# Optimization experiments

Hardware: AMD Instinct MI355X
Metric: run time of the kernel (lower is better)

## Reference

```python
import jax, jax.numpy as jnp
import numpy as np

BITS = 4
GROUP = 128
MAXQ = 2 ** BITS - 1  # 15 for asymmetric 4-bit


def round_ste(x):
    # straight-through rounding: round in fwd, identity in bwd
    return x + jax.lax.stop_gradient(jnp.round(x) - x)


def quant_weight(weight, v, min_scale, max_scale):
    """Groupwise asymmetric fake-quant (quantize + dequantize) of weight.

    weight: [O, I], v: [O, I] learnable rounding offsets,
    min_scale/max_scale: [O*I/GROUP] learnable min/max scales in [-1, 0].
    """
    O, I = weight.shape
    w = weight.reshape(-1, GROUP)          # [G, GROUP]
    vv = v.reshape(-1, GROUP)              # [G, GROUP]
    wmin_t = jnp.minimum(w.min(axis=1), 0.0)  # [G]
    wmax_t = jnp.maximum(w.max(axis=1), 0.0)  # [G]
    # forward clamps min/max scale into [-1, 0] before use
    wmin = wmin_t * (jnp.clip(min_scale, -1.0, 0.0) + 1.0)
    wmax = wmax_t * (jnp.clip(max_scale, -1.0, 0.0) + 1.0)
    degenerate = (wmin == 0.0) & (wmax == 0.0)
    wmin = jnp.where(degenerate, -1.0, wmin)
    wmax = jnp.where(degenerate, 1.0, wmax)
    # scale stored at fp16 precision (scale_dtype), then used in fp32 math
    scale = ((wmax - wmin) / MAXQ).astype(jnp.float16).astype(weight.dtype)  # [G]
    zp = round_ste(-wmin / scale)                                            # [G]
    int_w = round_ste(w / scale[:, None] + vv)                               # [G, GROUP]
    q = jnp.clip(int_w + zp[:, None], 0.0, float(MAXQ))
    wq = scale[:, None] * (q - zp[:, None])
    return wq.reshape(O, I)


def setup_inputs() -> dict:
    key = jax.random.key(0)
    k_x, k_w, k_b, k_v = jax.random.split(key, 4)
    O, I = 4096, 4096
    B, S = 2, 2048
    x = jax.random.normal(k_x, (B, S, I), dtype=jnp.float32)
    weight = jax.random.normal(k_w, (O, I), dtype=jnp.float32) * 0.02
    bias = jax.random.normal(k_b, (O,), dtype=jnp.float32) * 0.02
    value = jax.random.normal(k_v, (O, I), dtype=jnp.float32) * 0.1
    n_groups = O * I // GROUP
    min_scale = jnp.zeros((n_groups,), dtype=jnp.float32)
    max_scale = jnp.zeros((n_groups,), dtype=jnp.float32)
    return {"x": x, "weight": weight, "bias": bias, "value": value,
            "min_scale": min_scale, "max_scale": max_scale}


def reference(x, weight, bias, value, min_scale, max_scale):
    wq = quant_weight(weight, value, min_scale, max_scale)  # [O, I]
    # F.linear(x, weight_q, bias): x @ wq.T + bias
    return jnp.einsum('bsi,oi->bso', x, wq) + bias
```

## Files before the change

### kernel.cpp

```cpp
#include <hip/hip_runtime.h>
#include <hip/hip_bf16.h>
#include <hip/hip_fp16.h>
#include <stdint.h>

#define M_DIM 4096
#define N_DIM 4096
#define K_DIM 4096
#define GROUPSZ 128
#define MAXQ 15.0f

#define BM 256
#define BN 256
#define BK 64
#define T_TILES (K_DIM / BK)

typedef __attribute__((ext_vector_type(8))) short short8;
typedef __attribute__((ext_vector_type(4))) float f32x4;

__global__ __launch_bounds__(256) void quant_kernel(
    const float* __restrict__ weight, const float* __restrict__ value,
    const float* __restrict__ min_scale, const float* __restrict__ max_scale,
    __hip_bfloat16* __restrict__ wq)
{
    const int tid  = threadIdx.x;
    const int wave = tid >> 6;
    const int lane = tid & 63;
    const long g    = (long)blockIdx.x * 4 + wave;
    const long base = g * GROUPSZ + lane * 2;

    const float2 w = *(const float2*)(weight + base);
    const float2 v = *(const float2*)(value  + base);

    float mn = fminf(w.x, w.y);
    float mx = fmaxf(w.x, w.y);
#pragma unroll
    for (int off = 32; off >= 1; off >>= 1) {
        mn = fminf(mn, __shfl_xor(mn, off, 64));
        mx = fmaxf(mx, __shfl_xor(mx, off, 64));
    }
    mn = fminf(mn, 0.0f);
    mx = fmaxf(mx, 0.0f);

    const float ms = fminf(fmaxf(min_scale[g], -1.0f), 0.0f) + 1.0f;
    const float xs = fminf(fmaxf(max_scale[g], -1.0f), 0.0f) + 1.0f;
    float wmin = mn * ms;
    float wmax = mx * xs;
    if (wmin == 0.0f && wmax == 0.0f) { wmin = -1.0f; wmax = 1.0f; }

    const float scale = (float)(_Float16)((wmax - wmin) / MAXQ);
    const float zp    = rintf(-wmin / scale);

    const float q0 = fminf(fmaxf(rintf(w.x / scale + v.x) + zp, 0.0f), MAXQ);
    const float q1 = fminf(fmaxf(rintf(w.y / scale + v.y) + zp, 0.0f), MAXQ);
    const float o0 = scale * (q0 - zp);
    const float o1 = scale * (q1 - zp);

    __hip_bfloat162 o;
    o.x = __float2bfloat16(o0);
    o.y = __float2bfloat16(o1);
    *(__hip_bfloat162*)(wq + base) = o;
}

__global__ __launch_bounds__(256) void cast_kernel(
    const float* __restrict__ x, __hip_bfloat16* __restrict__ xb)
{
    const long i = ((long)blockIdx.x * 256 + threadIdx.x) * 8;
    const float4 a = *(const float4*)(x + i);
    const float4 b = *(const float4*)(x + i + 4);
    union { short8 s; __hip_bfloat16 h[8]; } u;
    u.h[0] = __float2bfloat16(a.x);
    u.h[1] = __float2bfloat16(a.y);
    u.h[2] = __float2bfloat16(a.z);
    u.h[3] = __float2bfloat16(a.w);
    u.h[4] = __float2bfloat16(b.x);
    u.h[5] = __float2bfloat16(b.y);
    u.h[6] = __float2bfloat16(b.z);
    u.h[7] = __float2bfloat16(b.w);
    *(short8*)(xb + i) = u.s;
}

__global__ __launch_bounds__(512, 2) void gemm_kernel(
    const __hip_bfloat16* __restrict__ A,
    const __hip_bfloat16* __restrict__ B,
    const float* __restrict__ bias,
    float* __restrict__ C)
{
    __shared__ __align__(16) char lds[131072];

    const int tid  = threadIdx.x;
    const int lane = tid & 63;
    const int wv   = tid >> 6;
    const int wm   = wv >> 2;
    const int wn   = wv & 3;

    const int bid = blockIdx.x;
    const int swz = (bid & 7) * (gridDim.x >> 3) + (bid >> 3);
    const int brow = (swz >> 4) * BM;
    const int bcol = (swz & 15) * BN;

    const int stg_r = tid >> 3;
    const int cc    = ((tid & 7) ^ (stg_r & 7)) * 8;

#define STAGE(XP, rowbase, h, tau, ldsbase)                                         \
    { _Pragma("unroll")                                                             \
      for (int inst = 0; inst < 2; ++inst) {                                        \
        const __hip_bfloat16* g = (XP) +                                            \
            (size_t)((rowbase) + (h) * 128 + inst * 64 + stg_r) * K_DIM +           \
            (tau) * 64 + cc;                                                        \
        __builtin_amdgcn_global_load_lds(                                           \
            (const __attribute__((address_space(1))) void*)g,                       \
            (__attribute__((address_space(3))) void*)(lds + (ldsbase) +             \
                (h) * 16384 + inst * 8192 + (wv << 10)),                            \
            16, 0, 0);                                                              \
      } }

    const int ro = lane & 15;
    const int hi = lane >> 4;
    const int slot0 = ((0 + hi) ^ (ro & 7)) << 4;
    const int slot1 = ((4 + hi) ^ (ro & 7)) << 4;
    const int rbA = (wm * 128 + ro) * 128;
    const int rbB = (wn * 64  + ro) * 128;

    f32x4 acc[8][4] = {};

    STAGE(B, bcol, 0, 0, 65536);
    STAGE(B, bcol, 1, 0, 65536);
    STAGE(A, brow, 0, 0, 0);
    STAGE(A, brow, 1, 0, 0);
    STAGE(B, bcol, 0, 1, 65536 + 32768);
    STAGE(B, bcol, 1, 1, 65536 + 32768);
    asm volatile("s_waitcnt vmcnt(4)" ::: "memory");
    __builtin_amdgcn_s_barrier();

#define MFMA16(M0, XA0, XA1)                                                        \
    { _Pragma("unroll")                                                             \
      for (int n = 0; n < 4; ++n) {                                                 \
        acc[M0][n]     = __builtin_amdgcn_mfma_f32_16x16x32_bf16((XA0)[0], bfr[n][0], acc[M0][n],     0, 0, 0); \
        acc[M0 + 1][n] = __builtin_amdgcn_mfma_f32_16x16x32_bf16((XA1)[0], bfr[n][0], acc[M0 + 1][n], 0, 0, 0); \
      }                                                                             \
      _Pragma("unroll")                                                             \
      for (int n = 0; n < 4; ++n) {                                                 \
        acc[M0][n]     = __builtin_amdgcn_mfma_f32_16x16x32_bf16((XA0)[1], bfr[n][1], acc[M0][n],     0, 0, 0); \
        acc[M0 + 1][n] = __builtin_amdgcn_mfma_f32_16x16x32_bf16((XA1)[1], bfr[n][1], acc[M0 + 1][n], 0, 0, 0); \
      } }

#define LD_A(dst, m)                                                                \
    dst[0] = *(const short8*)(bA + (m) * 2048 + slot0);                             \
    dst[1] = *(const short8*)(bA + (m) * 2048 + slot1);

    for (int t = 0; t < T_TILES; ++t) {
        const int c = t & 1;
        const char* bA = lds + c * 32768 + rbA;
        const char* bB = lds + 65536 + c * 32768 + rbB;

        short8 bfr[4][2];
        short8 x0[2], x1[2];

#pragma unroll
        for (int n = 0; n < 4; ++n) {
            bfr[n][0] = *(const short8*)(bB + n * 2048 + slot0);
            bfr[n][1] = *(const short8*)(bB + n * 2048 + slot1);
        }
        LD_A(x0, 0); LD_A(x1, 1);
        if (t + 1 < T_TILES) {
            STAGE(A, brow, 0, t + 1, (c ^ 1) * 32768);
            STAGE(A, brow, 1, t + 1, (c ^ 1) * 32768);
        }
        asm volatile("s_waitcnt lgkmcnt(8)" ::: "memory");
        __builtin_amdgcn_s_barrier();
        asm volatile("s_waitcnt lgkmcnt(0)" ::: "memory");
        __builtin_amdgcn_s_setprio(1);
        MFMA16(0, x0, x1);
        __builtin_amdgcn_s_setprio(0);
        __builtin_amdgcn_s_barrier();

        LD_A(x0, 2); LD_A(x1, 3);
        if (t + 2 < T_TILES) { STAGE(B, bcol, 0, t + 2, 65536 + c * 32768); }
        __builtin_amdgcn_s_barrier();
        asm volatile("s_waitcnt lgkmcnt(0)" ::: "memory");
        __builtin_amdgcn_s_setprio(1);
        MFMA16(2, x0, x1);
        __builtin_amdgcn_s_setprio(0);
        __builtin_amdgcn_s_barrier();

        LD_A(x0, 4); LD_A(x1, 5);
        if (t + 2 < T_TILES) { STAGE(B, bcol, 1, t + 2, 65536 + c * 32768); }
        __builtin_amdgcn_s_barrier();
        asm volatile("s_waitcnt lgkmcnt(0)" ::: "memory");
        __builtin_amdgcn_s_setprio(1);
        MFMA16(4, x0, x1);
        __builtin_amdgcn_s_setprio(0);
        __builtin_amdgcn_s_barrier();

        LD_A(x0, 6); LD_A(x1, 7);
        if (t < T_TILES - 2) { asm volatile("s_waitcnt vmcnt(4)" ::: "memory"); }
        else                 { asm volatile("s_waitcnt vmcnt(0)" ::: "memory"); }
        __builtin_amdgcn_s_barrier();
        asm volatile("s_waitcnt lgkmcnt(0)" ::: "memory");
        __builtin_amdgcn_s_setprio(1);
        MFMA16(6, x0, x1);
        __builtin_amdgcn_s_setprio(0);
        __builtin_amdgcn_s_barrier();
    }

    const int col   = lane & 15;
    const int rbase = hi * 4;
    float bv[4];
#pragma unroll
    for (int n = 0; n < 4; ++n)
        bv[n] = bias[bcol + wn * 64 + n * 16 + col];

#pragma unroll
    for (int m = 0; m < 8; ++m) {
        const int mrow = brow + wm * 128 + m * 16 + rbase;
#pragma unroll
        for (int r = 0; r < 4; ++r) {
            float* crow = C + (size_t)(mrow + r) * N_DIM + bcol + wn * 64 + col;
#pragma unroll
            for (int n = 0; n < 4; ++n)
                crow[n * 16] = acc[m][n][r] + bv[n];
        }
    }
#undef STAGE
#undef MFMA16
#undef LD_A
}

extern "C" void kernel_launch(void* const* d_in, const int* in_sizes, int n_in,
                              void* d_out, int out_size, void* d_ws, size_t ws_size,
                              hipStream_t stream) {
    const float* x         = (const float*)d_in[0];
    const float* weight    = (const float*)d_in[1];
    const float* bias      = (const float*)d_in[2];
    const float* value     = (const float*)d_in[3];
    const float* min_scale = (const float*)d_in[4];
    const float* max_scale = (const float*)d_in[5];
    float* out = (float*)d_out;

    __hip_bfloat16* xb  = (__hip_bfloat16*)d_ws;
    __hip_bfloat16* wqb = xb + (size_t)M_DIM * K_DIM;

    quant_kernel<<<(N_DIM * K_DIM / GROUPSZ) / 4, 256, 0, stream>>>(
        weight, value, min_scale, max_scale, wqb);
    cast_kernel<<<(M_DIM * K_DIM) / (256 * 8), 256, 0, stream>>>(x, xb);
    gemm_kernel<<<(M_DIM / BM) * (N_DIM / BN), 512, 0, stream>>>(xb, wqb, bias, out);
}
```

Baseline: 172.3 us.

## Software-pipeline LDS fragment loads across MFMA phases with register double buffering

Restructures the GEMM main loop so that the B fragments and first A fragments for the next K tile are read from LDS during the current tile's last MFMA phase. The A fragments for each phase are loaded one phase ahead. The loop is unrolled by two with ping-pong register sets, and several barriers and full lgkmcnt(0) waits are replaced by partial waits. The goal is to hide LDS read latency behind MFMA work and cut synchronisation stalls. The cost is higher VGPR pressure and more fragile waitcnt and barrier ordering around the async global-to-LDS stages.

```diff
diff --git a/kernel.cpp b/kernel.cpp
--- a/kernel.cpp
+++ b/kernel.cpp
@@ -122,6 +122,24 @@
     const int rbB = (wn * 64  + ro) * 128;
 
     f32x4 acc[8][4] = {};
+    short8 bR0[4][2], bR1[4][2];
+    short8 aP0[2][2], aP1[2][2];
+
+#define MFMA16(M0, BIN, X0, X1)                                                     \
+    { _Pragma("unroll")                                                             \
+      for (int n = 0; n < 4; ++n) {                                                 \
+        acc[M0][n]     = __builtin_amdgcn_mfma_f32_16x16x32_bf16((X0)[0], BIN[n][0], acc[M0][n],     0, 0, 0); \
+        acc[M0 + 1][n] = __builtin_amdgcn_mfma_f32_16x16x32_bf16((X1)[0], BIN[n][0], acc[M0 + 1][n], 0, 0, 0); \
+      }                                                                             \
+      _Pragma("unroll")                                                             \
+      for (int n = 0; n < 4; ++n) {                                                 \
+        acc[M0][n]     = __builtin_amdgcn_mfma_f32_16x16x32_bf16((X0)[1], BIN[n][1], acc[M0][n],     0, 0, 0); \
+        acc[M0 + 1][n] = __builtin_amdgcn_mfma_f32_16x16x32_bf16((X1)[1], BIN[n][1], acc[M0 + 1][n], 0, 0, 0); \
+      } }
+
+#define LDA2(dst, m)                                                                \
+    dst[0] = *(const short8*)(bA_ + (m) * 2048 + slot0);                            \
+    dst[1] = *(const short8*)(bA_ + (m) * 2048 + slot1);
 
     STAGE(B, bcol, 0, 0, 65536);
     STAGE(B, bcol, 1, 0, 65536);
@@ -131,76 +149,76 @@
     STAGE(B, bcol, 1, 1, 65536 + 32768);
     asm volatile("s_waitcnt vmcnt(4)" ::: "memory");
     __builtin_amdgcn_s_barrier();
-
-#define MFMA16(M0, XA0, XA1)                                                        \
-    { _Pragma("unroll")                                                             \
-      for (int n = 0; n < 4; ++n) {                                                 \
-        acc[M0][n]     = __builtin_amdgcn_mfma_f32_16x16x32_bf16((XA0)[0], bfr[n][0], acc[M0][n],     0, 0, 0); \
-        acc[M0 + 1][n] = __builtin_amdgcn_mfma_f32_16x16x32_bf16((XA1)[0], bfr[n][0], acc[M0 + 1][n], 0, 0, 0); \
-      }                                                                             \
-      _Pragma("unroll")                                                             \
-      for (int n = 0; n < 4; ++n) {                                                 \
-        acc[M0][n]     = __builtin_amdgcn_mfma_f32_16x16x32_bf16((XA0)[1], bfr[n][1], acc[M0][n],     0, 0, 0); \
-        acc[M0 + 1][n] = __builtin_amdgcn_mfma_f32_16x16x32_bf16((XA1)[1], bfr[n][1], acc[M0 + 1][n], 0, 0, 0); \
-      } }
-
-#define LD_A(dst, m)                                                                \
-    dst[0] = *(const short8*)(bA + (m) * 2048 + slot0);                             \
-    dst[1] = *(const short8*)(bA + (m) * 2048 + slot1);
-
-    for (int t = 0; t < T_TILES; ++t) {
-        const int c = t & 1;
-        const char* bA = lds + c * 32768 + rbA;
-        const char* bB = lds + 65536 + c * 32768 + rbB;
-
-        short8 bfr[4][2];
-        short8 x0[2], x1[2];
-
+    {
+        const char* bB_ = lds + 65536 + rbB;
+        const char* bA_ = lds + rbA;
 #pragma unroll
         for (int n = 0; n < 4; ++n) {
-            bfr[n][0] = *(const short8*)(bB + n * 2048 + slot0);
-            bfr[n][1] = *(const short8*)(bB + n * 2048 + slot1);
+            bR0[n][0] = *(const short8*)(bB_ + n * 2048 + slot0);
+            bR0[n][1] = *(const short8*)(bB_ + n * 2048 + slot1);
         }
-        LD_A(x0, 0); LD_A(x1, 1);
-        if (t + 1 < T_TILES) {
-            STAGE(A, brow, 0, t + 1, (c ^ 1) * 32768);
-            STAGE(A, brow, 1, t + 1, (c ^ 1) * 32768);
-        }
-        asm volatile("s_waitcnt lgkmcnt(8)" ::: "memory");
-        __builtin_amdgcn_s_barrier();
-        asm volatile("s_waitcnt lgkmcnt(0)" ::: "memory");
-        __builtin_amdgcn_s_setprio(1);
-        MFMA16(0, x0, x1);
-        __builtin_amdgcn_s_setprio(0);
-        __builtin_amdgcn_s_barrier();
-
-        LD_A(x0, 2); LD_A(x1, 3);
-        if (t + 2 < T_TILES) { STAGE(B, bcol, 0, t + 2, 65536 + c * 32768); }
-        __builtin_amdgcn_s_barrier();
-        asm volatile("s_waitcnt lgkmcnt(0)" ::: "memory");
-        __builtin_amdgcn_s_setprio(1);
-        MFMA16(2, x0, x1);
-        __builtin_amdgcn_s_setprio(0);
-        __builtin_amdgcn_s_barrier();
-
-        LD_A(x0, 4); LD_A(x1, 5);
-        if (t + 2 < T_TILES) { STAGE(B, bcol, 1, t + 2, 65536 + c * 32768); }
-        __builtin_amdgcn_s_barrier();
-        asm volatile("s_waitcnt lgkmcnt(0)" ::: "memory");
-        __builtin_amdgcn_s_setprio(1);
-        MFMA16(4, x0, x1);
-        __builtin_amdgcn_s_setprio(0);
-        __builtin_amdgcn_s_barrier();
-
-        LD_A(x0, 6); LD_A(x1, 7);
-        if (t < T_TILES - 2) { asm volatile("s_waitcnt vmcnt(4)" ::: "memory"); }
-        else                 { asm volatile("s_waitcnt vmcnt(0)" ::: "memory"); }
-        __builtin_amdgcn_s_barrier();
-        asm volatile("s_waitcnt lgkmcnt(0)" ::: "memory");
-        __builtin_amdgcn_s_setprio(1);
-        MFMA16(6, x0, x1);
-        __builtin_amdgcn_s_setprio(0);
-        __builtin_amdgcn_s_barrier();
+        LDA2(aP0[0], 0); LDA2(aP0[1], 1);
+    }
+
+#define TILE_BODY(T_, BIN, BOUT, AIN, AOUT)                                         \
+    {                                                                               \
+        const int t_ = (T_);                                                        \
+        const int c_ = t_ & 1;                                                      \
+        const char* bA_  = lds + c_ * 32768 + rbA;                                  \
+        const char* bAn_ = lds + (c_ ^ 1) * 32768 + rbA;                            \
+        const char* bBn_ = lds + 65536 + (c_ ^ 1) * 32768 + rbB;                    \
+        short8 a23[2][2], a45[2][2], a67[2][2];                                     \
+                                                                            \
+        LDA2(a23[0], 2); LDA2(a23[1], 3);                                           \
+        if (t_ + 1 < T_TILES) {                                                     \
+            STAGE(A, brow, 0, t_ + 1, (c_ ^ 1) * 32768);                            \
+            STAGE(A, brow, 1, t_ + 1, (c_ ^ 1) * 32768);                            \
+        }                                                                           \
+        asm volatile("s_waitcnt lgkmcnt(4)" ::: "memory");                          \
+        __builtin_amdgcn_s_setprio(1);                                              \
+        MFMA16(0, BIN, AIN[0], AIN[1]);                                             \
+        __builtin_amdgcn_s_setprio(0);                                              \
+        __builtin_amdgcn_s_barrier();                                               \
+                                                                            \
+        LDA2(a45[0], 4); LDA2(a45[1], 5);                                           \
+        if (t_ + 2 < T_TILES) { STAGE(B, bcol, 0, t_ + 2, 65536 + c_ * 32768); }    \
+        asm volatile("s_waitcnt lgkmcnt(4)" ::: "memory");                          \
+        __builtin_amdgcn_s_setprio(1);                                              \
+        MFMA16(2, BIN, a23[0], a23[1]);                                             \
+        __builtin_amdgcn_s_setprio(0);                                              \
+        __builtin_amdgcn_s_barrier();                                               \
+                                                                            \
+        LDA2(a67[0], 6); LDA2(a67[1], 7);                                           \
+        if (t_ + 2 < T_TILES) { STAGE(B, bcol, 1, t_ + 2, 65536 + c_ * 32768); }    \
+        asm volatile("s_waitcnt lgkmcnt(4)" ::: "memory");                          \
+        __builtin_amdgcn_s_setprio(1);                                              \
+        MFMA16(4, BIN, a45[0], a45[1]);                                             \
+        __builtin_amdgcn_s_setprio(0);                                              \
+        if (t_ + 2 < T_TILES)      { asm volatile("s_waitcnt vmcnt(4)" ::: "memory"); } \
+        else if (t_ + 1 < T_TILES) { asm volatile("s_waitcnt vmcnt(0)" ::: "memory"); } \
+        __builtin_amdgcn_s_barrier();                                               \
+                                                                            \
+        if (t_ + 1 < T_TILES) {                                                     \
+            _Pragma("unroll")                                                       \
+            for (int n = 0; n < 4; ++n) {                                           \
+                BOUT[n][0] = *(const short8*)(bBn_ + n * 2048 + slot0);             \
+                BOUT[n][1] = *(const short8*)(bBn_ + n * 2048 + slot1);             \
+            }                                                                       \
+            { const char* bA_ = bAn_;                                               \
+              LDA2(AOUT[0], 0); LDA2(AOUT[1], 1); }                                 \
+            asm volatile("s_waitcnt lgkmcnt(12)" ::: "memory");                     \
+        } else {                                                                    \
+            asm volatile("s_waitcnt lgkmcnt(0)" ::: "memory");                      \
+        }                                                                           \
+        __builtin_amdgcn_s_setprio(1);                                              \
+        MFMA16(6, BIN, a67[0], a67[1]);                                             \
+        __builtin_amdgcn_s_setprio(0);                                              \
+        __builtin_amdgcn_s_barrier();                                               \
+    }
+
+    for (int tt = 0; tt < T_TILES; tt += 2) {
+        TILE_BODY(tt,     bR0, bR1, aP0, aP1);
+        TILE_BODY(tt + 1, bR1, bR0, aP1, aP0);
     }
 
     const int col   = lane & 15;
@@ -223,7 +241,8 @@
     }
 #undef STAGE
 #undef MFMA16
-#undef LD_A
+#undef LDA2
+#undef TILE_BODY
 }
 
 extern "C" void kernel_launch(void* const* d_in, const int* in_sizes, int n_in,
```

Result: slower. 342.9 us (+99.0%).

## Restructure GEMM main loop to one barrier per K-tile with pipelined LDS reads

Applied to the files above, without the earlier changes.

Replaces the eight barriers per K-tile with a single vmcnt(0)-plus-barrier at the top of each iteration. A and B for the next tile are now staged together into the alternate buffer, so B is prefetched one tile ahead instead of two. LDS fragment reads for each next sub-block are issued before the MFMAs of the current one, using separate register sets, partial lgkmcnt waits and sched_barrier fences, and the loop is forced to unroll 1. This aims to cut synchronization stalls and overlap LDS reads with MFMA, at the cost of a shallower global prefetch whose full vmcnt(0) wait may expose memory latency, plus higher register pressure.

```diff
diff --git a/kernel.cpp b/kernel.cpp
--- a/kernel.cpp
+++ b/kernel.cpp
@@ -123,84 +123,79 @@
 
     f32x4 acc[8][4] = {};
 
+#define MFMA16(M0, X0, X1)                                                          \
+    { _Pragma("unroll")                                                             \
+      for (int n = 0; n < 4; ++n) {                                                 \
+        acc[M0][n]     = __builtin_amdgcn_mfma_f32_16x16x32_bf16((X0)[0], bfr[n][0], acc[M0][n],     0, 0, 0); \
+        acc[M0 + 1][n] = __builtin_amdgcn_mfma_f32_16x16x32_bf16((X1)[0], bfr[n][0], acc[M0 + 1][n], 0, 0, 0); \
+      }                                                                             \
+      _Pragma("unroll")                                                             \
+      for (int n = 0; n < 4; ++n) {                                                 \
+        acc[M0][n]     = __builtin_amdgcn_mfma_f32_16x16x32_bf16((X0)[1], bfr[n][1], acc[M0][n],     0, 0, 0); \
+        acc[M0 + 1][n] = __builtin_amdgcn_mfma_f32_16x16x32_bf16((X1)[1], bfr[n][1], acc[M0 + 1][n], 0, 0, 0); \
+      } }
+
+#define LDA2(dst, m)                                                                \
+    dst[0] = *(const short8*)(bA + (m) * 2048 + slot0);                             \
+    dst[1] = *(const short8*)(bA + (m) * 2048 + slot1);
+
     STAGE(B, bcol, 0, 0, 65536);
     STAGE(B, bcol, 1, 0, 65536);
     STAGE(A, brow, 0, 0, 0);
     STAGE(A, brow, 1, 0, 0);
-    STAGE(B, bcol, 0, 1, 65536 + 32768);
-    STAGE(B, bcol, 1, 1, 65536 + 32768);
-    asm volatile("s_waitcnt vmcnt(4)" ::: "memory");
-    __builtin_amdgcn_s_barrier();
-
-#define MFMA16(M0, XA0, XA1)                                                        \
-    { _Pragma("unroll")                                                             \
-      for (int n = 0; n < 4; ++n) {                                                 \
-        acc[M0][n]     = __builtin_amdgcn_mfma_f32_16x16x32_bf16((XA0)[0], bfr[n][0], acc[M0][n],     0, 0, 0); \
-        acc[M0 + 1][n] = __builtin_amdgcn_mfma_f32_16x16x32_bf16((XA1)[0], bfr[n][0], acc[M0 + 1][n], 0, 0, 0); \
-      }                                                                             \
-      _Pragma("unroll")                                                             \
-      for (int n = 0; n < 4; ++n) {                                                 \
-        acc[M0][n]     = __builtin_amdgcn_mfma_f32_16x16x32_bf16((XA0)[1], bfr[n][1], acc[M0][n],     0, 0, 0); \
-        acc[M0 + 1][n] = __builtin_amdgcn_mfma_f32_16x16x32_bf16((XA1)[1], bfr[n][1], acc[M0 + 1][n], 0, 0, 0); \
-      } }
-
-#define LD_A(dst, m)                                                                \
-    dst[0] = *(const short8*)(bA + (m) * 2048 + slot0);                             \
-    dst[1] = *(const short8*)(bA + (m) * 2048 + slot1);
-
+
+#pragma unroll 1
     for (int t = 0; t < T_TILES; ++t) {
         const int c = t & 1;
         const char* bA = lds + c * 32768 + rbA;
         const char* bB = lds + 65536 + c * 32768 + rbB;
 
+        asm volatile("s_waitcnt vmcnt(0)" ::: "memory");
+        __builtin_amdgcn_s_barrier();
+
         short8 bfr[4][2];
-        short8 x0[2], x1[2];
+        short8 a0[2][2], a1[2][2], a2[2][2], a3[2][2];
 
 #pragma unroll
         for (int n = 0; n < 4; ++n) {
             bfr[n][0] = *(const short8*)(bB + n * 2048 + slot0);
             bfr[n][1] = *(const short8*)(bB + n * 2048 + slot1);
         }
-        LD_A(x0, 0); LD_A(x1, 1);
+        LDA2(a0[0], 0); LDA2(a0[1], 1);
+
         if (t + 1 < T_TILES) {
             STAGE(A, brow, 0, t + 1, (c ^ 1) * 32768);
             STAGE(A, brow, 1, t + 1, (c ^ 1) * 32768);
+            STAGE(B, bcol, 0, t + 1, 65536 + (c ^ 1) * 32768);
+            STAGE(B, bcol, 1, t + 1, 65536 + (c ^ 1) * 32768);
         }
-        asm volatile("s_waitcnt lgkmcnt(8)" ::: "memory");
-        __builtin_amdgcn_s_barrier();
+
+        LDA2(a1[0], 2); LDA2(a1[1], 3);
+        asm volatile("s_waitcnt lgkmcnt(4)" ::: "memory");
+        __builtin_amdgcn_sched_barrier(0);
+        __builtin_amdgcn_s_setprio(1);
+        MFMA16(0, a0[0], a0[1]);
+        __builtin_amdgcn_s_setprio(0);
+
+        LDA2(a2[0], 4); LDA2(a2[1], 5);
+        asm volatile("s_waitcnt lgkmcnt(4)" ::: "memory");
+        __builtin_amdgcn_sched_barrier(0);
+        __builtin_amdgcn_s_setprio(1);
+        MFMA16(2, a1[0], a1[1]);
+        __builtin_amdgcn_s_setprio(0);
+
+        LDA2(a3[0], 6); LDA2(a3[1], 7);
+        asm volatile("s_waitcnt lgkmcnt(4)" ::: "memory");
+        __builtin_amdgcn_sched_barrier(0);
+        __builtin_amdgcn_s_setprio(1);
+        MFMA16(4, a2[0], a2[1]);
+        __builtin_amdgcn_s_setprio(0);
+
         asm volatile("s_waitcnt lgkmcnt(0)" ::: "memory");
-        __builtin_amdgcn_s_setprio(1);
-        MFMA16(0, x0, x1);
-        __builtin_amdgcn_s_setprio(0);
-        __builtin_amdgcn_s_barrier();
-
-        LD_A(x0, 2); LD_A(x1, 3);
-        if (t + 2 < T_TILES) { STAGE(B, bcol, 0, t + 2, 65536 + c * 32768); }
-        __builtin_amdgcn_s_barrier();
-        asm volatile("s_waitcnt lgkmcnt(0)" ::: "memory");
-        __builtin_amdgcn_s_setprio(1);
-        MFMA16(2, x0, x1);
-        __builtin_amdgcn_s_setprio(0);
-        __builtin_amdgcn_s_barrier();
-
-        LD_A(x0, 4); LD_A(x1, 5);
-        if (t + 2 < T_TILES) { STAGE(B, bcol, 1, t + 2, 65536 + c * 32768); }
-        __builtin_amdgcn_s_barrier();
-        asm volatile("s_waitcnt lgkmcnt(0)" ::: "memory");
-        __builtin_amdgcn_s_setprio(1);
-        MFMA16(4, x0, x1);
-        __builtin_amdgcn_s_setprio(0);
-        __builtin_amdgcn_s_barrier();
-
-        LD_A(x0, 6); LD_A(x1, 7);
-        if (t < T_TILES - 2) { asm volatile("s_waitcnt vmcnt(4)" ::: "memory"); }
-        else                 { asm volatile("s_waitcnt vmcnt(0)" ::: "memory"); }
-        __builtin_amdgcn_s_barrier();
-        asm volatile("s_waitcnt lgkmcnt(0)" ::: "memory");
-        __builtin_amdgcn_s_setprio(1);
-        MFMA16(6, x0, x1);
-        __builtin_amdgcn_s_setprio(0);
-        __builtin_amdgcn_s_barrier();
+        __builtin_amdgcn_sched_barrier(0);
+        __builtin_amdgcn_s_setprio(1);
+        MFMA16(6, a3[0], a3[1]);
+        __builtin_amdgcn_s_setprio(0);
     }
 
     const int col   = lane & 15;
@@ -223,7 +218,7 @@
     }
 #undef STAGE
 #undef MFMA16
-#undef LD_A
+#undef LDA2
 }
 
 extern "C" void kernel_launch(void* const* d_in, const int* in_sizes, int n_in,
```

Measured after the change: 167.9 us. -2.6%, faster.
